# Kernel optimization log

Measured on AMD Instinct MI355X. Metric: run time of the kernel, lower is better.

The kernel has to match this reference:

```python
import jax, jax.numpy as jnp
import numpy as np

GAMMA = 20.0
NUM_VIEWS = 64

def setup_inputs() -> dict:
    key = jax.random.key(0)
    k1, k2, k3 = jax.random.split(key, 3)
    B, L, D = 16, 4096, 1024
    v_pad = jax.random.normal(k1, (B, L, D), dtype=jnp.float32)
    v_len = jax.random.randint(k2, (B,), 1, L + 1, dtype=jnp.int32)
    # (T, H, W) per sample; only W/H ratio matters -> square 64x64 grid
    grid_thws = jnp.tile(jnp.array([[1, 64, 64]], dtype=jnp.int32), (B, 1))
    centers = jax.random.uniform(k3, (B, NUM_VIEWS, 2), dtype=jnp.float32)
    return {"v_pad": v_pad, "v_len": v_len, "grid_thws": grid_thws, "centers": centers}

def reference(v_pad, v_len, grid_thws, centers):
    B, L, D = v_pad.shape
    Lv = v_len.astype(jnp.float32)                      # [B]
    H = grid_thws[:, 1].astype(jnp.float32)
    W = grid_thws[:, 2].astype(jnp.float32)
    # adaptive 2D mapping of the 1D token sequence
    W_eff = jnp.maximum(1, jnp.round(jnp.sqrt(Lv * (W / H))).astype(jnp.int32))  # [B]
    H_eff = jnp.maximum(1, jnp.ceil(Lv / W_eff.astype(jnp.float32)).astype(jnp.int32))
    idx = jnp.arange(L, dtype=jnp.int32)                # [L]
    We = W_eff[:, None]
    He = H_eff[:, None]
    x = (idx[None, :] % We).astype(jnp.float32) / We.astype(jnp.float32)   # [B, L]
    y = (idx[None, :] // We).astype(jnp.float32) / He.astype(jnp.float32)  # [B, L]
    coords = jnp.stack([x, y], axis=-1)                 # [B, L, 2]
    # squared distance from each view center to each token coord
    diff = centers[:, :, None, :] - coords[:, None, :, :]   # [B, V, L, 2]
    dist_sq = jnp.sum(diff * diff, axis=-1)                 # [B, V, L]
    valid = (idx[None, :] < v_len[:, None]).astype(v_pad.dtype)  # [B, L]
    m = jnp.exp(-GAMMA * dist_sq) * valid[:, None, :]       # [B, V, L]
    numerator = jnp.einsum('bvl,bld->bvd', m, v_pad)        # [B, V, D]
    denominator = jnp.sum(m, axis=-1, keepdims=True) + 1e-6 # [B, V, 1]
    return numerator / denominator
```

## Files before the change

kernel.cpp:

```cpp
#include <hip/hip_runtime.h>
#include <hip/hip_bf16.h>
#include <math.h>
#include <stdint.h>


constexpr int VV    = 64;
constexpr int DC    = 128;
constexpr int KS    = 64;
constexpr int NTH   = 256;
constexpr int ST2   = 134;
constexpr int CHUNK = 256;

typedef __attribute__((ext_vector_type(8))) short short8;
typedef __attribute__((ext_vector_type(4))) float f32x4;

static __device__ __forceinline__ unsigned short f2bf(float f) {
    __hip_bfloat16 h = __float2bfloat16(f);
    return __builtin_bit_cast(unsigned short, h);
}

__global__ __launch_bounds__(NTH)
void dvs_mfma(const float* __restrict__ v_pad, const int* __restrict__ v_len,
              const int* __restrict__ grid_thws, const float* __restrict__ centers,
              float* __restrict__ num_part,
              float* __restrict__ den_part,
              int B, int L, int D, int NKC)
{
    const int kc = blockIdx.x, dcb = blockIdx.y, b = blockIdx.z;
    const int Lv = v_len[b];
    const int l0 = kc * CHUNK;
    if (l0 >= Lv) return;
    const int l1 = min(l0 + CHUNK, Lv);

    const int tid  = threadIdx.x;
    const int d0   = dcb * DC;
    const int lane = tid & 63;
    const int wave = tid >> 6;

    __shared__ __align__(16) unsigned short smA[8 * 64 * 8];
    __shared__ __align__(16) unsigned short smB[KS][ST2];
    __shared__ float2 sxy[CHUNK];
    __shared__ float  sden[4][VV];

    const float Hf = (float)grid_thws[b*3 + 1];
    const float Wf = (float)grid_thws[b*3 + 2];
    const float sq = sqrtf((float)Lv * (Wf / Hf));
    int W_eff = (int)rintf(sq);                       if (W_eff < 1) W_eff = 1;
    int H_eff = (int)ceilf((float)Lv / (float)W_eff); if (H_eff < 1) H_eff = 1;
    const float invW = 1.f / (float)W_eff, invH = 1.f / (float)H_eff;

    const int    av  = tid & 63;
    const int    aq  = tid >> 6;
    const float2 ctr = ((const float2*)centers)[(size_t)b * VV + av];
    const int    amf = av >> 4, ar = av & 15;
    float denacc = 0.f;

    const int sd   = tid & 31;
    const int srow = tid >> 5;

    const int fcol = lane & 15, foct = lane >> 4;

    f32x4 acc[4][2];
#pragma unroll
    for (int i = 0; i < 4; ++i) {
        acc[i][0] = f32x4{0.f, 0.f, 0.f, 0.f};
        acc[i][1] = f32x4{0.f, 0.f, 0.f, 0.f};
    }

    const float* vp_b = v_pad + (size_t)b * L * D + d0;

    float4 ld[8];
#pragma unroll
    for (int it = 0; it < 8; ++it) {
        const int l = l0 + it * 8 + srow;
        ld[it] = make_float4(0.f, 0.f, 0.f, 0.f);
        if (l < l1)
            ld[it] = *(const float4*)(vp_b + (size_t)l * D + sd * 4);
    }
    if (tid < l1 - l0) {
        const int l   = l0 + tid;
        const int row = l / W_eff;
        const int col = l - row * W_eff;
        sxy[tid] = make_float2((float)col * invW, (float)row * invH);
    }
    __syncthreads();

    for (int lt = l0; lt < l1; lt += KS) {
#pragma unroll
        for (int it = 0; it < 8; ++it) {
            const int lrow = it * 8 + srow;
            unsigned* w = (unsigned*)&smB[lrow][sd * 4];
            w[0] = (unsigned)f2bf(ld[it].x) | ((unsigned)f2bf(ld[it].y) << 16);
            w[1] = (unsigned)f2bf(ld[it].z) | ((unsigned)f2bf(ld[it].w) << 16);
        }
#pragma unroll
        for (int ks = 0; ks < 2; ++ks) {
            union { unsigned short h[8]; short8 s; } ap;
#pragma unroll
            for (int j = 0; j < 8; ++j) {
                const int kl = ks * 32 + aq * 8 + j;
                const int l  = lt + kl;
                float m = 0.f;
                if (l < l1) {
                    const float2 xy = sxy[(lt - l0) + kl];
                    const float dx = ctr.x - xy.x, dy = ctr.y - xy.y;
                    m = __expf(-20.f * (dx * dx + dy * dy));
                }
                denacc += m;
                ap.h[j] = f2bf(m);
            }
            ((short8*)smA)[(ks * 4 + amf) * 64 + aq * 16 + ar] = ap.s;
        }
        __syncthreads();

        const int ltn = lt + KS;
        if (ltn < l1) {
#pragma unroll
            for (int it = 0; it < 8; ++it) {
                const int l = ltn + it * 8 + srow;
                ld[it] = make_float4(0.f, 0.f, 0.f, 0.f);
                if (l < l1)
                    ld[it] = *(const float4*)(vp_b + (size_t)l * D + sd * 4);
            }
        }

#pragma unroll
        for (int ks = 0; ks < 2; ++ks) {
            short8 af[4];
#pragma unroll
            for (int mf = 0; mf < 4; ++mf)
                af[mf] = ((const short8*)smA)[(ks * 4 + mf) * 64 + lane];

#pragma unroll
            for (int nf = 0; nf < 2; ++nf) {
                const int colx  = wave * 32 + nf * 16 + fcol;
                const int kbase = ks * 32 + foct * 8;
                union { unsigned short h[8]; short8 s; } bf;
#pragma unroll
                for (int j = 0; j < 8; ++j)
                    bf.h[j] = smB[kbase + j][colx];
#pragma unroll
                for (int mf = 0; mf < 4; ++mf)
                    acc[mf][nf] = __builtin_amdgcn_mfma_f32_16x16x32_bf16(
                        af[mf], bf.s, acc[mf][nf], 0, 0, 0);
            }
        }
        __syncthreads();
    }

    sden[aq][av] = denacc;
    __syncthreads();
    if (dcb == 0 && tid < VV) {
        den_part[((size_t)b * NKC + kc) * VV + tid] =
            sden[0][tid] + sden[1][tid] + sden[2][tid] + sden[3][tid];
    }

    float* basep = num_part + ((size_t)b * NKC + kc) * VV * (size_t)D + d0 + wave * 32;
#pragma unroll
    for (int mf = 0; mf < 4; ++mf) {
#pragma unroll
        for (int nf = 0; nf < 2; ++nf) {
            const int colx = nf * 16 + fcol;
            const int row0 = mf * 16 + foct * 4;
#pragma unroll
            for (int r = 0; r < 4; ++r)
                basep[(size_t)(row0 + r) * D + colx] = acc[mf][nf][r];
        }
    }
}

__global__ __launch_bounds__(256)
void dvs_reduce(const float* __restrict__ num_part,
                const float* __restrict__ den_part,
                const int*   __restrict__ v_len,
                float*       __restrict__ out,
                int B, int D, int NKC, int total4)
{
    const int idx = blockIdx.x * 256 + threadIdx.x;
    if (idx >= total4) return;
    const int dq4 = D / 4;
    const int d4  = idx % dq4;
    const int bv  = idx / dq4;
    const int b   = bv / VV;
    const int v   = bv - b * VV;

    const int nk = (v_len[b] + CHUNK - 1) / CHUNK;

    float  den = 1e-6f;
    float4 num = make_float4(0.f, 0.f, 0.f, 0.f);
    for (int k = 0; k < nk; ++k) {
        den += den_part[((size_t)b * NKC + k) * VV + v];
        const float4 p = ((const float4*)(num_part +
                          (((size_t)b * NKC + k) * VV + v) * (size_t)D))[d4];
        num.x += p.x; num.y += p.y; num.z += p.z; num.w += p.w;
    }
    const float inv = 1.0f / den;
    ((float4*)out)[(size_t)bv * dq4 + d4] =
        make_float4(num.x * inv, num.y * inv, num.z * inv, num.w * inv);
}

extern "C" void kernel_launch(void* const* d_in, const int* in_sizes, int n_in,
                              void* d_out, int out_size, void* d_ws, size_t ws_size,
                              hipStream_t stream)
{
    const float* v_pad     = (const float*)d_in[0];
    const int*   v_len     = (const int*)d_in[1];
    const int*   grid_thws = (const int*)d_in[2];
    const float* centers   = (const float*)d_in[3];
    float*       out       = (float*)d_out;

    const int B = in_sizes[1];
    const int D = out_size / (B * VV);
    const int L = in_sizes[0] / (B * D);
    const int NKC = (L + CHUNK - 1) / CHUNK;

    float* num_part = (float*)d_ws;
    float* den_part = num_part + (size_t)B * NKC * VV * D;

    dim3 grid1(NKC, D / DC, B);
    dvs_mfma<<<grid1, NTH, 0, stream>>>(v_pad, v_len, grid_thws, centers,
                                        num_part, den_part, B, L, D, NKC);

    const int total4 = B * VV * D / 4;
    dvs_reduce<<<(total4 + 255) / 256, 256, 0, stream>>>(num_part, den_part,
                                                         v_len, out, B, D, NKC,
                                                         total4);
}
```

Baseline: 46.10 us.

## Precompute bf16 weight tiles in a prep kernel and balance L-chunks per sample

```diff
diff --git a/kernel.cpp b/kernel.cpp
--- a/kernel.cpp
+++ b/kernel.cpp
@@ -4,12 +4,12 @@
 #include <stdint.h>
 
 
-constexpr int VV    = 64;
-constexpr int DC    = 128;
-constexpr int KS    = 64;
-constexpr int NTH   = 256;
-constexpr int ST2   = 134;
-constexpr int CHUNK = 256;
+constexpr int VV  = 64;
+constexpr int DC  = 128;
+constexpr int KS  = 64;
+constexpr int NTH = 256;
+constexpr int ST2 = 134;
+constexpr int KCH = 8;
 
 typedef __attribute__((ext_vector_type(8))) short short8;
 typedef __attribute__((ext_vector_type(4))) float f32x4;
@@ -19,45 +19,97 @@
     return __builtin_bit_cast(unsigned short, h);
 }
 
+__global__ __launch_bounds__(256)
+void dvs_prep(const int* __restrict__ v_len, const int* __restrict__ gthw,
+              const float* __restrict__ centers,
+              unsigned short* __restrict__ mws,
+              float* __restrict__ den_tile,
+              int NT)
+{
+    const int t = blockIdx.x, b = blockIdx.y;
+    const int Lv = v_len[b];
+    const int lt = t * KS;
+    if (lt >= Lv) return;
+
+    const float Hf = (float)gthw[b*3 + 1];
+    const float Wf = (float)gthw[b*3 + 2];
+    const float sq = sqrtf((float)Lv * (Wf / Hf));
+    int W_eff = (int)rintf(sq);                       if (W_eff < 1) W_eff = 1;
+    int H_eff = (int)ceilf((float)Lv / (float)W_eff); if (H_eff < 1) H_eff = 1;
+    const float invW = 1.f / (float)W_eff, invH = 1.f / (float)H_eff;
+
+    const int tid  = threadIdx.x;
+    const int lane = tid & 63, wave = tid >> 6;
+    const int ar = lane & 15, koct = lane >> 4;
+
+    __shared__ float sden[2][4][VV];
+
+    short8* mtile = (short8*)mws + ((size_t)b * NT + t) * 8 * 64;
+
+#pragma unroll
+    for (int i = 0; i < 2; ++i) {
+        const int f  = wave * 2 + i;
+        const int ks = f >> 2, mf = f & 3;
+        const int v  = mf * 16 + ar;
+        const float2 ctr = ((const float2*)centers)[(size_t)b * VV + v];
+
+        int l   = lt + ks * 32 + koct * 8;
+        int row = l / W_eff;
+        int col = l - row * W_eff;
+        float y = (float)row * invH;
+
+        union { unsigned short h[8]; short8 s; } ap;
+        float ds = 0.f;
+#pragma unroll
+        for (int j = 0; j < 8; ++j) {
+            float m = 0.f;
+            if (l + j < Lv) {
+                const float x  = (float)col * invW;
+                const float dx = ctr.x - x, dy = ctr.y - y;
+                m = __expf(-20.f * (dx * dx + dy * dy));
+            }
+            ds += m;
+            ap.h[j] = f2bf(m);
+            if (++col == W_eff) { col = 0; ++row; y = (float)row * invH; }
+        }
+        mtile[f * 64 + lane] = ap.s;
+        sden[ks][koct][v] = ds;
+    }
+    __syncthreads();
+    if (tid < VV) {
+        float s = 0.f;
+#pragma unroll
+        for (int ks = 0; ks < 2; ++ks)
+#pragma unroll
+            for (int q = 0; q < 4; ++q) s += sden[ks][q][tid];
+        den_tile[((size_t)b * NT + t) * VV + tid] = s;
+    }
+}
+
 __global__ __launch_bounds__(NTH)
 void dvs_mfma(const float* __restrict__ v_pad, const int* __restrict__ v_len,
-              const int* __restrict__ grid_thws, const float* __restrict__ centers,
+              const unsigned short* __restrict__ mws,
+              const float* __restrict__ den_tile,
               float* __restrict__ num_part,
               float* __restrict__ den_part,
-              int B, int L, int D, int NKC)
-{
-    const int kc = blockIdx.x, dcb = blockIdx.y, b = blockIdx.z;
+              int L, int D, int NT)
+{
+    const int kblk = blockIdx.x, dcb = blockIdx.y, b = blockIdx.z;
     const int Lv = v_len[b];
-    const int l0 = kc * CHUNK;
+    const int chunk = (((Lv + KCH - 1) / KCH) + 63) & ~63;
+    const int l0 = kblk * chunk;
     if (l0 >= Lv) return;
-    const int l1 = min(l0 + CHUNK, Lv);
+    const int l1 = min(l0 + chunk, Lv);
 
     const int tid  = threadIdx.x;
     const int d0   = dcb * DC;
     const int lane = tid & 63;
     const int wave = tid >> 6;
 
-    __shared__ __align__(16) unsigned short smA[8 * 64 * 8];
     __shared__ __align__(16) unsigned short smB[KS][ST2];
-    __shared__ float2 sxy[CHUNK];
-    __shared__ float  sden[4][VV];
-
-    const float Hf = (float)grid_thws[b*3 + 1];
-    const float Wf = (float)grid_thws[b*3 + 2];
-    const float sq = sqrtf((float)Lv * (Wf / Hf));
-    int W_eff = (int)rintf(sq);                       if (W_eff < 1) W_eff = 1;
-    int H_eff = (int)ceilf((float)Lv / (float)W_eff); if (H_eff < 1) H_eff = 1;
-    const float invW = 1.f / (float)W_eff, invH = 1.f / (float)H_eff;
-
-    const int    av  = tid & 63;
-    const int    aq  = tid >> 6;
-    const float2 ctr = ((const float2*)centers)[(size_t)b * VV + av];
-    const int    amf = av >> 4, ar = av & 15;
-    float denacc = 0.f;
 
     const int sd   = tid & 31;
     const int srow = tid >> 5;
-
     const int fcol = lane & 15, foct = lane >> 4;
 
     f32x4 acc[4][2];
@@ -66,8 +118,11 @@
         acc[i][0] = f32x4{0.f, 0.f, 0.f, 0.f};
         acc[i][1] = f32x4{0.f, 0.f, 0.f, 0.f};
     }
-
-    const float* vp_b = v_pad + (size_t)b * L * D + d0;
+    float denacc = 0.f;
+
+    const float*  vp_b   = v_pad + (size_t)b * L * D + d0;
+    const short8* mws_b  = (const short8*)mws + (size_t)b * NT * 8 * 64;
+    const float*  dt_b   = den_tile + (size_t)b * NT * VV;
 
     float4 ld[8];
 #pragma unroll
@@ -77,13 +132,6 @@
         if (l < l1)
             ld[it] = *(const float4*)(vp_b + (size_t)l * D + sd * 4);
     }
-    if (tid < l1 - l0) {
-        const int l   = l0 + tid;
-        const int row = l / W_eff;
-        const int col = l - row * W_eff;
-        sxy[tid] = make_float2((float)col * invW, (float)row * invH);
-    }
-    __syncthreads();
 
     for (int lt = l0; lt < l1; lt += KS) {
 #pragma unroll
@@ -92,24 +140,6 @@
             unsigned* w = (unsigned*)&smB[lrow][sd * 4];
             w[0] = (unsigned)f2bf(ld[it].x) | ((unsigned)f2bf(ld[it].y) << 16);
             w[1] = (unsigned)f2bf(ld[it].z) | ((unsigned)f2bf(ld[it].w) << 16);
-        }
-#pragma unroll
-        for (int ks = 0; ks < 2; ++ks) {
-            union { unsigned short h[8]; short8 s; } ap;
-#pragma unroll
-            for (int j = 0; j < 8; ++j) {
-                const int kl = ks * 32 + aq * 8 + j;
-                const int l  = lt + kl;
-                float m = 0.f;
-                if (l < l1) {
-                    const float2 xy = sxy[(lt - l0) + kl];
-                    const float dx = ctr.x - xy.x, dy = ctr.y - xy.y;
-                    m = __expf(-20.f * (dx * dx + dy * dy));
-                }
-                denacc += m;
-                ap.h[j] = f2bf(m);
-            }
-            ((short8*)smA)[(ks * 4 + amf) * 64 + aq * 16 + ar] = ap.s;
         }
         __syncthreads();
 
@@ -124,13 +154,19 @@
             }
         }
 
+        const short8* mt = mws_b + ((size_t)(lt >> 6)) * 8 * 64;
+        short8 af[2][4];
+#pragma unroll
+        for (int ks = 0; ks < 2; ++ks)
+#pragma unroll
+            for (int mf = 0; mf < 4; ++mf)
+                af[ks][mf] = mt[(ks * 4 + mf) * 64 + lane];
+
+        if (dcb == 0 && tid < VV)
+            denacc += dt_b[(size_t)(lt >> 6) * VV + tid];
+
 #pragma unroll
         for (int ks = 0; ks < 2; ++ks) {
-            short8 af[4];
-#pragma unroll
-            for (int mf = 0; mf < 4; ++mf)
-                af[mf] = ((const short8*)smA)[(ks * 4 + mf) * 64 + lane];
-
 #pragma unroll
             for (int nf = 0; nf < 2; ++nf) {
                 const int colx  = wave * 32 + nf * 16 + fcol;
@@ -142,20 +178,16 @@
 #pragma unroll
                 for (int mf = 0; mf < 4; ++mf)
                     acc[mf][nf] = __builtin_amdgcn_mfma_f32_16x16x32_bf16(
-                        af[mf], bf.s, acc[mf][nf], 0, 0, 0);
+                        af[ks][mf], bf.s, acc[mf][nf], 0, 0, 0);
             }
         }
         __syncthreads();
     }
 
-    sden[aq][av] = denacc;
-    __syncthreads();
-    if (dcb == 0 && tid < VV) {
-        den_part[((size_t)b * NKC + kc) * VV + tid] =
-            sden[0][tid] + sden[1][tid] + sden[2][tid] + sden[3][tid];
-    }
-
-    float* basep = num_part + ((size_t)b * NKC + kc) * VV * (size_t)D + d0 + wave * 32;
+    if (dcb == 0 && tid < VV)
+        den_part[((size_t)b * KCH + kblk) * VV + tid] = denacc;
+
+    float* basep = num_part + ((size_t)b * KCH + kblk) * VV * (size_t)D + d0 + wave * 32;
 #pragma unroll
     for (int mf = 0; mf < 4; ++mf) {
 #pragma unroll
@@ -174,7 +206,7 @@
                 const float* __restrict__ den_part,
                 const int*   __restrict__ v_len,
                 float*       __restrict__ out,
-                int B, int D, int NKC, int total4)
+                int D, int total4)
 {
     const int idx = blockIdx.x * 256 + threadIdx.x;
     if (idx >= total4) return;
@@ -184,14 +216,16 @@
     const int b   = bv / VV;
     const int v   = bv - b * VV;
 
-    const int nk = (v_len[b] + CHUNK - 1) / CHUNK;
+    const int Lv    = v_len[b];
+    const int chunk = (((Lv + KCH - 1) / KCH) + 63) & ~63;
+    const int nk    = (Lv + chunk - 1) / chunk;
 
     float  den = 1e-6f;
     float4 num = make_float4(0.f, 0.f, 0.f, 0.f);
     for (int k = 0; k < nk; ++k) {
-        den += den_part[((size_t)b * NKC + k) * VV + v];
+        den += den_part[((size_t)b * KCH + k) * VV + v];
         const float4 p = ((const float4*)(num_part +
-                          (((size_t)b * NKC + k) * VV + v) * (size_t)D))[d4];
+                          (((size_t)b * KCH + k) * VV + v) * (size_t)D))[d4];
         num.x += p.x; num.y += p.y; num.z += p.z; num.w += p.w;
     }
     const float inv = 1.0f / den;
@@ -209,20 +243,25 @@
     const float* centers   = (const float*)d_in[3];
     float*       out       = (float*)d_out;
 
-    const int B = in_sizes[1];
-    const int D = out_size / (B * VV);
-    const int L = in_sizes[0] / (B * D);
-    const int NKC = (L + CHUNK - 1) / CHUNK;
-
-    float* num_part = (float*)d_ws;
-    float* den_part = num_part + (size_t)B * NKC * VV * D;
-
-    dim3 grid1(NKC, D / DC, B);
-    dvs_mfma<<<grid1, NTH, 0, stream>>>(v_pad, v_len, grid_thws, centers,
-                                        num_part, den_part, B, L, D, NKC);
+    const int B  = in_sizes[1];
+    const int D  = out_size / (B * VV);
+    const int L  = in_sizes[0] / (B * D);
+    const int NT = (L + KS - 1) / KS;
+
+    float*          num_part = (float*)d_ws;
+    float*          den_part = num_part + (size_t)B * KCH * VV * D;
+    float*          den_tile = den_part + (size_t)B * KCH * VV;
+    unsigned short* mws      = (unsigned short*)(den_tile + (size_t)B * NT * VV);
+
+    dim3 gridP(NT, B);
+    dvs_prep<<<gridP, 256, 0, stream>>>(v_len, grid_thws, centers, mws,
+                                        den_tile, NT);
+
+    dim3 gridG(KCH, D / DC, B);
+    dvs_mfma<<<gridG, NTH, 0, stream>>>(v_pad, v_len, mws, den_tile,
+                                        num_part, den_part, L, D, NT);
 
     const int total4 = B * VV * D / 4;
     dvs_reduce<<<(total4 + 255) / 256, 256, 0, stream>>>(num_part, den_part,
-                                                         v_len, out, B, D, NKC,
-                                                         total4);
-}
+                                                         v_len, out, D, total4);
+}
```

Measured after the change: 42.77 us. 7.2% less time.
